# Kernel optimization log

Measured on AMD Instinct MI355X. Metric: run time of the kernel, lower is better.

## Reference

```python
import jax, jax.numpy as jnp
import numpy as np

N = 50000       # nodes
E = 800000      # edges (before self-loops)
NFEAT = 256
NHID = 64
NHEADS = 4
NOUT = 256
NEG_SLOPE = 0.2
BN_EPS = 1e-5
LN_EPS = 1e-5


def setup_inputs() -> dict:
    key = jax.random.key(0)
    ks = jax.random.split(key, 12)
    g = lambda k, s: (jax.random.normal(k, s, dtype=jnp.float32) * 0.05)
    inp = {
        "x": jax.random.normal(ks[0], (N, NFEAT), dtype=jnp.float32),
        "edge_index": jax.random.randint(ks[1], (2, E), 0, N, dtype=jnp.int32),
        # layer 1: GATConv(NFEAT, NHID, heads=NHEADS, concat=True)
        "W1": g(ks[2], (NFEAT, NHEADS * NHID)),
        "att_src1": g(ks[3], (NHEADS, NHID)),
        "att_dst1": g(ks[4], (NHEADS, NHID)),
        "bias1": jnp.zeros((NHEADS * NHID,), jnp.float32),
        # layer 2: GATConv(NHEADS*NHID, NOUT, heads=1, concat=False)
        "W2": g(ks[5], (NHEADS * NHID, NOUT)),
        "att_src2": g(ks[6], (1, NOUT)),
        "att_dst2": g(ks[7], (1, NOUT)),
        "bias2": jnp.zeros((NOUT,), jnp.float32),
        # BatchNorm1d (eval mode: running stats)
        "bn_gamma": jnp.ones((NOUT,), jnp.float32),
        "bn_beta": jnp.zeros((NOUT,), jnp.float32),
        "bn_mean": g(ks[8], (NOUT,)),
        "bn_var": jnp.ones((NOUT,), jnp.float32),
        # LayerNorm
        "ln_gamma": jnp.ones((NOUT,), jnp.float32),
        "ln_beta": jnp.zeros((NOUT,), jnp.float32),
    }
    return inp


def _gat_conv(x, edge_index, W, att_src, att_dst, bias, concat):
    """PyG-style GATConv (eval mode, add_self_loops=True)."""
    n = x.shape[0]
    H, C = att_src.shape
    xp = (x @ W).reshape(n, H, C)                    # [N,H,C]
    loop = jnp.arange(n, dtype=edge_index.dtype)
    src = jnp.concatenate([edge_index[0], loop])     # message source j
    dst = jnp.concatenate([edge_index[1], loop])     # aggregation target i
    a_src = jnp.einsum("nhc,hc->nh", xp, att_src)    # [N,H]
    a_dst = jnp.einsum("nhc,hc->nh", xp, att_dst)
    e = jax.nn.leaky_relu(a_src[src] + a_dst[dst], NEG_SLOPE)  # [Etot,H]
    # segment softmax over edges sharing the same dst
    m = jax.ops.segment_max(e, dst, num_segments=n)
    e = jnp.exp(e - m[dst])
    denom = jax.ops.segment_sum(e, dst, num_segments=n)
    alpha = e / (denom[dst] + 1e-16)                 # [Etot,H]
    out = jax.ops.segment_sum(alpha[:, :, None] * xp[src], dst, num_segments=n)  # [N,H,C]
    out = out.reshape(n, H * C) if concat else out.mean(axis=1)
    return out + bias


def reference(x, edge_index, W1, att_src1, att_dst1, bias1,
              W2, att_src2, att_dst2, bias2,
              bn_gamma, bn_beta, bn_mean, bn_var, ln_gamma, ln_beta):
    # eval mode: F.dropout is identity
    h = jax.nn.elu(_gat_conv(x, edge_index, W1, att_src1, att_dst1, bias1, True))
    h = jax.nn.elu(_gat_conv(h, edge_index, W2, att_src2, att_dst2, bias2, False))
    # BatchNorm1d (eval: running stats)
    h = (h - bn_mean) * jax.lax.rsqrt(bn_var + BN_EPS) * bn_gamma + bn_beta
    # LayerNorm over last dim
    mu = h.mean(axis=-1, keepdims=True)
    var = jnp.mean((h - mu) ** 2, axis=-1, keepdims=True)
    h = (h - mu) * jax.lax.rsqrt(var + LN_EPS) * ln_gamma + ln_beta
    return h
```

## Files before the change

### kernel.cpp

```cpp
#include <hip/hip_runtime.h>
#include <cstddef>
#include <cstdint>

#define NNODES 50000
#define NEDGES 800000
#define FDIM   256

#define SCAN_BLOCKS 256
#define SCAN_CHUNK  ((NNODES + SCAN_BLOCKS - 1) / SCAN_BLOCKS)

typedef __attribute__((ext_vector_type(8))) _Float16 f16x8;
typedef __attribute__((ext_vector_type(8))) unsigned short ushort8;
typedef __attribute__((ext_vector_type(4))) float f32x4;

__device__ __forceinline__ float leaky_exp(float a) {
    float e = a > 0.f ? a : 0.2f * a;
    return __expf(e);
}
__device__ __forceinline__ unsigned short f2h(float f) {
    return __builtin_bit_cast(unsigned short, (_Float16)f);
}
__device__ __forceinline__ float hlo(uint32_t u) {
    _Float16 h = __builtin_bit_cast(_Float16, (unsigned short)(u & 0xffffu));
    return (float)h;
}
__device__ __forceinline__ float hhi(uint32_t u) {
    _Float16 h = __builtin_bit_cast(_Float16, (unsigned short)(u >> 16));
    return (float)h;
}
__device__ __forceinline__ float rlanef(float v, int l) {
    return __builtin_bit_cast(float,
        __builtin_amdgcn_readlane(__builtin_bit_cast(int, v), l));
}

__global__ __launch_bounds__(256) void wprep_k(const float* __restrict__ W1,
                                               unsigned short* __restrict__ Wt1,
                                               const float* __restrict__ W2,
                                               unsigned short* __restrict__ Wt2) {
    const float* W = blockIdx.y ? W2 : W1;
    unsigned short* Wt = blockIdx.y ? Wt2 : Wt1;
    int n = blockIdx.x, k = threadIdx.x;
    Wt[n * 256 + k] = f2h(W[k * 256 + n]);
}

template <bool AFP32, bool FUSE_LOGITS>
__global__ __launch_bounds__(256) void gemm_mfma(const void* __restrict__ Aab,
                                                 const unsigned short* __restrict__ Bt,
                                                 unsigned short* __restrict__ C,
                                                 const float* __restrict__ atts,
                                                 const float* __restrict__ attd,
                                                 float* __restrict__ as_,
                                                 float* __restrict__ ad_,
                                                 int M) {
    __shared__ unsigned short As[128 * 64];
    __shared__ unsigned short Bs[128 * 64];
    const int t = threadIdx.x;
    const int lane = t & 63, wid = t >> 6;
    const int wr = wid >> 1, wc = wid & 1;
    const int bm = blockIdx.x * 128;
    const int bny = blockIdx.y;
    const int bn = bny * 128;
    f32x4 acc[4][4] = {};
    const int lrow = t >> 3, lslot = t & 7;
    for (int k0 = 0; k0 < 256; k0 += 64) {
        __syncthreads();
#pragma unroll
        for (int i = 0; i < 4; ++i) {
            int row = lrow + 32 * i;
            int ga = bm + row; ga = ga < M ? ga : M - 1;
            if (AFP32) {
                const float* p = (const float*)Aab + (size_t)ga * FDIM + k0 + lslot * 8;
                float4 f0 = *(const float4*)p;
                float4 f1 = *(const float4*)(p + 4);
                ushort8 r;
                r[0] = f2h(f0.x); r[1] = f2h(f0.y); r[2] = f2h(f0.z); r[3] = f2h(f0.w);
                r[4] = f2h(f1.x); r[5] = f2h(f1.y); r[6] = f2h(f1.z); r[7] = f2h(f1.w);
                *(ushort8*)(As + row * 64 + ((lslot ^ (row & 7)) << 3)) = r;
            } else {
                const unsigned short* A16 = (const unsigned short*)Aab;
                uint4 av = *(const uint4*)(A16 + (size_t)ga * FDIM + k0 + lslot * 8);
                *(uint4*)(As + row * 64 + ((lslot ^ (row & 7)) << 3)) = av;
            }
            uint4 bv = *(const uint4*)(Bt + (size_t)(bn + row) * FDIM + k0 + lslot * 8);
            *(uint4*)(Bs + row * 64 + ((lslot ^ (row & 7)) << 3)) = bv;
        }
        __syncthreads();
#pragma unroll
        for (int ks = 0; ks < 2; ++ks) {
            const int kq = ks * 4 + (lane >> 4);
            f16x8 a[4], b[4];
#pragma unroll
            for (int f = 0; f < 4; ++f) {
                int ra = wr * 64 + f * 16 + (lane & 15);
                a[f] = *(const f16x8*)(As + ra * 64 + ((kq ^ (ra & 7)) << 3));
                int rb = wc * 64 + f * 16 + (lane & 15);
                b[f] = *(const f16x8*)(Bs + rb * 64 + ((kq ^ (rb & 7)) << 3));
            }
#pragma unroll
            for (int mf = 0; mf < 4; ++mf)
#pragma unroll
                for (int nf = 0; nf < 4; ++nf)
                    acc[mf][nf] = __builtin_amdgcn_mfma_f32_16x16x32_f16(
                        a[mf], b[nf], acc[mf][nf], 0, 0, 0);
        }
    }
    const int col0 = bn + wc * 64 + (lane & 15);
    const int row00 = bm + wr * 64 + (lane >> 4) * 4;
    if (FUSE_LOGITS) {
        const int head = 2 * bny + wc;
        float sv4[4], dv4[4];
#pragma unroll
        for (int nf = 0; nf < 4; ++nf) {
            sv4[nf] = atts[col0 + nf * 16];
            dv4[nf] = attd[col0 + nf * 16];
        }
#pragma unroll
        for (int mf = 0; mf < 4; ++mf)
#pragma unroll
            for (int r = 0; r < 4; ++r) {
                float ps = 0.f, pd = 0.f;
#pragma unroll
                for (int nf = 0; nf < 4; ++nf) {
                    float v = acc[mf][nf][r];
                    ps = fmaf(v, sv4[nf], ps);
                    pd = fmaf(v, dv4[nf], pd);
                }
#pragma unroll
                for (int off = 1; off < 16; off <<= 1) {
                    ps += __shfl_xor(ps, off);
                    pd += __shfl_xor(pd, off);
                }
                int row = row00 + mf * 16 + r;
                if ((lane & 15) == 0 && row < M) {
                    as_[row * 4 + head] = ps;
                    ad_[row * 4 + head] = pd;
                }
            }
    }
#pragma unroll
    for (int mf = 0; mf < 4; ++mf)
#pragma unroll
        for (int nf = 0; nf < 4; ++nf) {
            f32x4 v = acc[mf][nf];
            int col = col0 + nf * 16;
#pragma unroll
            for (int r = 0; r < 4; ++r) {
                int row = row00 + mf * 16 + r;
                if (row < M) C[(size_t)row * FDIM + col] = f2h(v[r]);
            }
        }
}

template <int H>
__global__ __launch_bounds__(256) void aprep_k(const unsigned short* __restrict__ xp,
                                               const float* __restrict__ atts,
                                               const float* __restrict__ attd,
                                               float* __restrict__ as_,
                                               float* __restrict__ ad_) {
    const int lane = threadIdx.x & 63;
    const int n = blockIdx.x * 4 + (threadIdx.x >> 6);
    if (n >= NNODES) return;
    const int c = lane << 2;
    uint2 u = *(const uint2*)(xp + (size_t)n * FDIM + c);
    float v0 = hlo(u.x), v1 = hhi(u.x), v2 = hlo(u.y), v3 = hhi(u.y);
    float4 s4 = *(const float4*)(atts + c);
    float4 d4 = *(const float4*)(attd + c);
    float ss = v0 * s4.x + v1 * s4.y + v2 * s4.z + v3 * s4.w;
    float sd = v0 * d4.x + v1 * d4.y + v2 * d4.z + v3 * d4.w;
    constexpr int G = 64 / H;
#pragma unroll
    for (int off = 1; off < G; off <<= 1) {
        ss += __shfl_xor(ss, off);
        sd += __shfl_xor(sd, off);
    }
    if ((lane & (G - 1)) == 0) {
        int h = lane / G;
        as_[n * H + h] = ss;
        ad_[n * H + h] = sd;
    }
}

__global__ __launch_bounds__(256) void hist_k(const int* __restrict__ ei,
                                              int* __restrict__ deg) {
    int e = blockIdx.x * 256 + threadIdx.x;
    if (e < NEDGES) atomicAdd(&deg[ei[NEDGES + e]], 1);
}

__global__ __launch_bounds__(256) void scanA_k(const int* __restrict__ deg,
                                               int* __restrict__ bsum) {
    const int b = blockIdx.x, t = threadIdx.x;
    const int i = b * SCAN_CHUNK + t;
    int v = (t < SCAN_CHUNK && i < NNODES) ? deg[i] : 0;
#pragma unroll
    for (int off = 1; off < 64; off <<= 1) v += __shfl_xor(v, off);
    __shared__ int ws[4];
    if ((t & 63) == 0) ws[t >> 6] = v;
    __syncthreads();
    if (t == 0) bsum[b] = ws[0] + ws[1] + ws[2] + ws[3];
}

__global__ __launch_bounds__(256) void scanB_k(const int* __restrict__ bsum,
                                               int* __restrict__ boff,
                                               int* __restrict__ rowptr) {
    const int t = threadIdx.x;
    const int lane = t & 63, wid = t >> 6;
    int orig = bsum[t];
    int v = orig;
#pragma unroll
    for (int off = 1; off < 64; off <<= 1) {
        int u = __shfl_up(v, off);
        if (lane >= off) v += u;
    }
    __shared__ int ws[4], wo[4];
    if (lane == 63) ws[wid] = v;
    __syncthreads();
    if (t == 0) {
        int a = 0;
        for (int k = 0; k < 4; ++k) { wo[k] = a; a += ws[k]; }
        rowptr[NNODES] = a;
    }
    __syncthreads();
    boff[t] = wo[wid] + v - orig;
}

__global__ __launch_bounds__(256) void scanC_k(const int* __restrict__ deg,
                                               const int* __restrict__ boff,
                                               int* __restrict__ rowptr) {
    const int b = blockIdx.x, t = threadIdx.x;
    const int i = b * SCAN_CHUNK + t;
    const bool ok = (t < SCAN_CHUNK && i < NNODES);
    int orig = ok ? deg[i] : 0;
    int v = orig;
    const int lane = t & 63, wid = t >> 6;
#pragma unroll
    for (int off = 1; off < 64; off <<= 1) {
        int u = __shfl_up(v, off);
        if (lane >= off) v += u;
    }
    __shared__ int ws[4], wo[4];
    if (lane == 63) ws[wid] = v;
    __syncthreads();
    if (t == 0) {
        int a = 0;
        for (int k = 0; k < 4; ++k) { wo[k] = a; a += ws[k]; }
    }
    __syncthreads();
    if (ok) rowptr[i] = boff[b] + wo[wid] + v - orig;
}

__global__ __launch_bounds__(256) void scatter_k(const int* __restrict__ ei,
                                                 const int* __restrict__ rowptr,
                                                 int* __restrict__ deg,
                                                 int* __restrict__ ssrc) {
    int e = blockIdx.x * 256 + threadIdx.x;
    if (e >= NEDGES) return;
    int s = ei[e], d = ei[NEDGES + e];
    int old = atomicSub(&deg[d], 1);
    ssrc[rowptr[d + 1] - old] = s;
}

__global__ __launch_bounds__(256) void gather1_k(const unsigned short* __restrict__ xp,
                                                 const float* __restrict__ as_,
                                                 const float* __restrict__ ad_,
                                                 const int* __restrict__ rowptr,
                                                 const int* __restrict__ ssrc,
                                                 const float* __restrict__ bias,
                                                 unsigned short* __restrict__ out) {
    const int lane = threadIdx.x & 63;
    const int n = blockIdx.x * 4 + (threadIdx.x >> 6);
    if (n >= NNODES) return;
    const int h = lane >> 4;
    const int c = lane << 2;
    const int eloc = lane >> 2;
    const int hh = lane & 3;
    const float adW = ad_[n * 4 + hh];
    float a0 = 0.f, a1 = 0.f, a2 = 0.f, a3 = 0.f, den = 0.f;
    const int beg = rowptr[n], end = rowptr[n + 1];
    for (int base = beg; base < end; base += 16) {
        int my_e = base + eloc;
        float wv = 0.f; int sv = 0;
        if (my_e < end) {
            sv = ssrc[my_e];
            wv = leaky_exp(as_[sv * 4 + hh] + adW);
        }
        float dred = wv;
#pragma unroll
        for (int off = 4; off < 64; off <<= 1) dred += __shfl_xor(dred, off);
        den += __shfl(dred, h);
        const int cnt = min(16, end - base);
        int e = 0;
        for (; e + 8 <= cnt; e += 8) {
            uint2 u[8]; float w[8];
#pragma unroll
            for (int q = 0; q < 8; ++q) {
                int sq = __builtin_amdgcn_readlane(sv, (e + q) << 2);
                u[q] = *(const uint2*)(xp + (((unsigned)sq << 8) + (unsigned)c));
                w[q] = __shfl(wv, ((e + q) << 2) | h);
            }
#pragma unroll
            for (int q = 0; q < 8; ++q) {
                a0 = fmaf(hlo(u[q].x), w[q], a0);
                a1 = fmaf(hhi(u[q].x), w[q], a1);
                a2 = fmaf(hlo(u[q].y), w[q], a2);
                a3 = fmaf(hhi(u[q].y), w[q], a3);
            }
        }
        for (; e < cnt; ++e) {
            int sq = __builtin_amdgcn_readlane(sv, e << 2);
            uint2 u0 = *(const uint2*)(xp + (((unsigned)sq << 8) + (unsigned)c));
            float w0 = __shfl(wv, (e << 2) | h);
            a0 = fmaf(hlo(u0.x), w0, a0); a1 = fmaf(hhi(u0.x), w0, a1);
            a2 = fmaf(hlo(u0.y), w0, a2); a3 = fmaf(hhi(u0.y), w0, a3);
        }
    }
    {
        float w = leaky_exp(as_[n * 4 + h] + ad_[n * 4 + h]);
        uint2 u = *(const uint2*)(xp + (((unsigned)n << 8) + (unsigned)c));
        a0 = fmaf(hlo(u.x), w, a0); a1 = fmaf(hhi(u.x), w, a1);
        a2 = fmaf(hlo(u.y), w, a2); a3 = fmaf(hhi(u.y), w, a3);
        den += w;
    }
    const float inv = 1.f / (den + 1e-16f);
    float4 b4 = *(const float4*)(bias + c);
    float o[4] = {a0 * inv + b4.x, a1 * inv + b4.y,
                  a2 * inv + b4.z, a3 * inv + b4.w};
#pragma unroll
    for (int j = 0; j < 4; ++j) o[j] = o[j] > 0.f ? o[j] : __expf(o[j]) - 1.f;
    ushort4 r;
    r.x = f2h(o[0]); r.y = f2h(o[1]); r.z = f2h(o[2]); r.w = f2h(o[3]);
    *(ushort4*)(out + (size_t)n * FDIM + c) = r;
}

__global__ __launch_bounds__(256) void gather2_k(const unsigned short* __restrict__ xp,
                                                 const float* __restrict__ as_,
                                                 const float* __restrict__ ad_,
                                                 const int* __restrict__ rowptr,
                                                 const int* __restrict__ ssrc,
                                                 const float* __restrict__ bias,
                                                 const float* __restrict__ bng,
                                                 const float* __restrict__ bnb,
                                                 const float* __restrict__ bnm,
                                                 const float* __restrict__ bnv,
                                                 const float* __restrict__ lng,
                                                 const float* __restrict__ lnb,
                                                 float* __restrict__ out) {
    const int lane = threadIdx.x & 63;
    const int n = blockIdx.x * 4 + (threadIdx.x >> 6);
    if (n >= NNODES) return;
    const int c = lane << 2;
    const float adn = ad_[n];
    float a0 = 0.f, a1 = 0.f, a2 = 0.f, a3 = 0.f, den = 0.f;
    const int beg = rowptr[n], end = rowptr[n + 1];
    for (int base = beg; base < end; base += 64) {
        int my_e = base + lane;
        float wv = 0.f; int sv = 0;
        if (my_e < end) {
            sv = ssrc[my_e];
            wv = leaky_exp(as_[sv] + adn);
        }
        float dred = wv;
#pragma unroll
        for (int off = 1; off < 64; off <<= 1) dred += __shfl_xor(dred, off);
        den += dred;
        const int cnt = min(64, end - base);
        int e = 0;
        for (; e + 8 <= cnt; e += 8) {
            uint2 u[8]; float w[8];
#pragma unroll
            for (int q = 0; q < 8; ++q) {
                int sq = __builtin_amdgcn_readlane(sv, e + q);
                u[q] = *(const uint2*)(xp + (((unsigned)sq << 8) + (unsigned)c));
                w[q] = rlanef(wv, e + q);
            }
#pragma unroll
            for (int q = 0; q < 8; ++q) {
                a0 = fmaf(hlo(u[q].x), w[q], a0);
                a1 = fmaf(hhi(u[q].x), w[q], a1);
                a2 = fmaf(hlo(u[q].y), w[q], a2);
                a3 = fmaf(hhi(u[q].y), w[q], a3);
            }
        }
        for (; e < cnt; ++e) {
            int sq = __builtin_amdgcn_readlane(sv, e);
            uint2 u0 = *(const uint2*)(xp + (((unsigned)sq << 8) + (unsigned)c));
            float w0 = rlanef(wv, e);
            a0 = fmaf(hlo(u0.x), w0, a0); a1 = fmaf(hhi(u0.x), w0, a1);
            a2 = fmaf(hlo(u0.y), w0, a2); a3 = fmaf(hhi(u0.y), w0, a3);
        }
    }
    {
        float w = leaky_exp(as_[n] + adn);
        uint2 u = *(const uint2*)(xp + (((unsigned)n << 8) + (unsigned)c));
        a0 = fmaf(hlo(u.x), w, a0); a1 = fmaf(hhi(u.x), w, a1);
        a2 = fmaf(hlo(u.y), w, a2); a3 = fmaf(hhi(u.y), w, a3);
        den += w;
    }
    const float inv = 1.f / (den + 1e-16f);
    float vals[4] = {a0 * inv, a1 * inv, a2 * inv, a3 * inv};
#pragma unroll
    for (int j = 0; j < 4; ++j) {
        float o = vals[j] + bias[c + j];
        o = o > 0.f ? o : __expf(o) - 1.f;
        o = (o - bnm[c + j]) * rsqrtf(bnv[c + j] + 1e-5f) * bng[c + j]
            + bnb[c + j];
        vals[j] = o;
    }
    float s1 = vals[0] + vals[1] + vals[2] + vals[3];
    float s2 = vals[0] * vals[0] + vals[1] * vals[1] +
               vals[2] * vals[2] + vals[3] * vals[3];
#pragma unroll
    for (int off = 1; off < 64; off <<= 1) {
        s1 += __shfl_xor(s1, off);
        s2 += __shfl_xor(s2, off);
    }
    float mu  = s1 * (1.f / 256.f);
    float var = s2 * (1.f / 256.f) - mu * mu;
    float r   = rsqrtf(var + 1e-5f);
#pragma unroll
    for (int j = 0; j < 4; ++j)
        out[(size_t)n * FDIM + c + j] = (vals[j] - mu) * r * lng[c + j] + lnb[c + j];
}

extern "C" void kernel_launch(void* const* d_in, const int* in_sizes, int n_in,
                              void* d_out, int out_size, void* d_ws, size_t ws_size,
                              hipStream_t stream) {
    const float* x      = (const float*)d_in[0];
    const int*   ei     = (const int*)d_in[1];
    const float* W1     = (const float*)d_in[2];
    const float* atts1  = (const float*)d_in[3];
    const float* attd1  = (const float*)d_in[4];
    const float* bias1  = (const float*)d_in[5];
    const float* W2     = (const float*)d_in[6];
    const float* atts2  = (const float*)d_in[7];
    const float* attd2  = (const float*)d_in[8];
    const float* bias2  = (const float*)d_in[9];
    const float* bng    = (const float*)d_in[10];
    const float* bnb    = (const float*)d_in[11];
    const float* bnm    = (const float*)d_in[12];
    const float* bnv    = (const float*)d_in[13];
    const float* lng    = (const float*)d_in[14];
    const float* lnb    = (const float*)d_in[15];

    const size_t NF = (size_t)NNODES * FDIM;
    unsigned short* xpbf = (unsigned short*)d_ws;
    unsigned short* xbf  = xpbf + NF;
    unsigned short* wt1  = xbf + NF;
    unsigned short* wt2  = wt1 + 65536;
    float* as1   = (float*)(wt2 + 65536);
    float* ad1   = as1 + (size_t)NNODES * 4;
    float* as2   = ad1 + (size_t)NNODES * 4;
    float* ad2   = as2 + NNODES;
    int*   deg    = (int*)(ad2 + NNODES);
    int*   rowptr = deg + NNODES;
    int*   bsum   = rowptr + (NNODES + 1);
    int*   boff   = bsum + SCAN_BLOCKS;
    int*   ssrc   = boff + SCAN_BLOCKS;
    float* outf  = (float*)d_out;

    const dim3 gemm_grid((NNODES + 127) / 128, 2);
    const int node_wave_blocks = (NNODES + 3) / 4;
    const int edge_thread_blocks = (NEDGES + 255) / 256;

    wprep_k<<<dim3(256, 2), 256, 0, stream>>>(W1, wt1, W2, wt2);
    hipMemsetAsync(deg, 0, NNODES * sizeof(int), stream);
    hist_k<<<edge_thread_blocks, 256, 0, stream>>>(ei, deg);
    scanA_k<<<SCAN_BLOCKS, 256, 0, stream>>>(deg, bsum);
    scanB_k<<<1, 256, 0, stream>>>(bsum, boff, rowptr);
    scanC_k<<<SCAN_BLOCKS, 256, 0, stream>>>(deg, boff, rowptr);
    scatter_k<<<edge_thread_blocks, 256, 0, stream>>>(ei, rowptr, deg, ssrc);

    gemm_mfma<true, true><<<gemm_grid, 256, 0, stream>>>(
        x, wt1, xpbf, atts1, attd1, as1, ad1, NNODES);
    gather1_k<<<node_wave_blocks, 256, 0, stream>>>(xpbf, as1, ad1, rowptr, ssrc,
                                                    bias1, xbf);

    gemm_mfma<false, false><<<gemm_grid, 256, 0, stream>>>(
        xbf, wt2, xpbf, nullptr, nullptr, nullptr, nullptr, NNODES);
    aprep_k<1><<<node_wave_blocks, 256, 0, stream>>>(xpbf, atts2, attd2, as2, ad2);
    gather2_k<<<node_wave_blocks, 256, 0, stream>>>(xpbf, as2, ad2, rowptr, ssrc,
                                                    bias2, bng, bnb, bnm, bnv,
                                                    lng, lnb, outf);
}
```

Before: 290.8 us.

## Slice feature matrices into 32-column planes and split gather per slice

Stores the projected features and hidden activations in a sliced layout of 32 columns per node plane, so each gather pass over one slice touches a smaller, more cache-friendly working set. Attention weights and softmax denominators are now computed once per edge in separate kernels and stored in buffers, one of which is placed in the output memory. The gather kernels then run over an 8-slice grid, each reading 4-byte chunks per neighbor. LayerNorm moves into a separate final kernel that reads fp16 intermediates. The cost is extra kernel launches, extra traffic for the weight buffers, and more index-load work repeated per slice.

```diff
diff --git a/kernel.cpp b/kernel.cpp
--- a/kernel.cpp
+++ b/kernel.cpp
@@ -27,10 +27,6 @@
 __device__ __forceinline__ float hhi(uint32_t u) {
     _Float16 h = __builtin_bit_cast(_Float16, (unsigned short)(u >> 16));
     return (float)h;
-}
-__device__ __forceinline__ float rlanef(float v, int l) {
-    return __builtin_bit_cast(float,
-        __builtin_amdgcn_readlane(__builtin_bit_cast(int, v), l));
 }
 
 __global__ __launch_bounds__(256) void wprep_k(const float* __restrict__ W1,
@@ -43,7 +39,7 @@
     Wt[n * 256 + k] = f2h(W[k * 256 + n]);
 }
 
-template <bool AFP32, bool FUSE_LOGITS>
+template <int AMODE, bool FUSE_LOGITS>
 __global__ __launch_bounds__(256) void gemm_mfma(const void* __restrict__ Aab,
                                                  const unsigned short* __restrict__ Bt,
                                                  unsigned short* __restrict__ C,
@@ -68,7 +64,7 @@
         for (int i = 0; i < 4; ++i) {
             int row = lrow + 32 * i;
             int ga = bm + row; ga = ga < M ? ga : M - 1;
-            if (AFP32) {
+            if (AMODE == 0) {
                 const float* p = (const float*)Aab + (size_t)ga * FDIM + k0 + lslot * 8;
                 float4 f0 = *(const float4*)p;
                 float4 f1 = *(const float4*)(p + 4);
@@ -78,7 +74,9 @@
                 *(ushort8*)(As + row * 64 + ((lslot ^ (row & 7)) << 3)) = r;
             } else {
                 const unsigned short* A16 = (const unsigned short*)Aab;
-                uint4 av = *(const uint4*)(A16 + (size_t)ga * FDIM + k0 + lslot * 8);
+                int k = k0 + lslot * 8;
+                uint4 av = *(const uint4*)(A16 +
+                    ((size_t)(k >> 5) * NNODES + ga) * 32 + (k & 31));
                 *(uint4*)(As + row * 64 + ((lslot ^ (row & 7)) << 3)) = av;
             }
             uint4 bv = *(const uint4*)(Bt + (size_t)(bn + row) * FDIM + k0 + lslot * 8);
@@ -142,42 +140,37 @@
 #pragma unroll
         for (int nf = 0; nf < 4; ++nf) {
             f32x4 v = acc[mf][nf];
-            int col = col0 + nf * 16;
+            int colb = bn + wc * 64 + nf * 16;
+            size_t base = (size_t)(colb >> 5) * NNODES * 32 + (colb & 31) + (lane & 15);
 #pragma unroll
             for (int r = 0; r < 4; ++r) {
                 int row = row00 + mf * 16 + r;
-                if (row < M) C[(size_t)row * FDIM + col] = f2h(v[r]);
+                if (row < M) C[base + (size_t)row * 32] = f2h(v[r]);
             }
         }
 }
 
-template <int H>
-__global__ __launch_bounds__(256) void aprep_k(const unsigned short* __restrict__ xp,
-                                               const float* __restrict__ atts,
-                                               const float* __restrict__ attd,
-                                               float* __restrict__ as_,
-                                               float* __restrict__ ad_) {
+__global__ __launch_bounds__(256) void aprep1_k(const unsigned short* __restrict__ xp_s,
+                                                const float* __restrict__ atts,
+                                                const float* __restrict__ attd,
+                                                float* __restrict__ as_,
+                                                float* __restrict__ ad_) {
     const int lane = threadIdx.x & 63;
     const int n = blockIdx.x * 4 + (threadIdx.x >> 6);
     if (n >= NNODES) return;
     const int c = lane << 2;
-    uint2 u = *(const uint2*)(xp + (size_t)n * FDIM + c);
+    uint2 u = *(const uint2*)(xp_s + ((size_t)(c >> 5) * NNODES + n) * 32 + (c & 31));
     float v0 = hlo(u.x), v1 = hhi(u.x), v2 = hlo(u.y), v3 = hhi(u.y);
     float4 s4 = *(const float4*)(atts + c);
     float4 d4 = *(const float4*)(attd + c);
     float ss = v0 * s4.x + v1 * s4.y + v2 * s4.z + v3 * s4.w;
     float sd = v0 * d4.x + v1 * d4.y + v2 * d4.z + v3 * d4.w;
-    constexpr int G = 64 / H;
-#pragma unroll
-    for (int off = 1; off < G; off <<= 1) {
+#pragma unroll
+    for (int off = 1; off < 64; off <<= 1) {
         ss += __shfl_xor(ss, off);
         sd += __shfl_xor(sd, off);
     }
-    if ((lane & (G - 1)) == 0) {
-        int h = lane / G;
-        as_[n * H + h] = ss;
-        ad_[n * H + h] = sd;
-    }
+    if (lane == 0) { as_[n] = ss; ad_[n] = sd; }
 }
 
 __global__ __launch_bounds__(256) void hist_k(const int* __restrict__ ei,
@@ -259,155 +252,224 @@
     ssrc[rowptr[d + 1] - old] = s;
 }
 
-__global__ __launch_bounds__(256) void gather1_k(const unsigned short* __restrict__ xp,
-                                                 const float* __restrict__ as_,
-                                                 const float* __restrict__ ad_,
-                                                 const int* __restrict__ rowptr,
-                                                 const int* __restrict__ ssrc,
-                                                 const float* __restrict__ bias,
-                                                 unsigned short* __restrict__ out) {
+__global__ __launch_bounds__(256) void wk1_k(const float* __restrict__ as_,
+                                             const float* __restrict__ ad_,
+                                             const int* __restrict__ rowptr,
+                                             const int* __restrict__ ssrc,
+                                             float* __restrict__ wbuf,
+                                             float* __restrict__ den,
+                                             float* __restrict__ wself) {
     const int lane = threadIdx.x & 63;
     const int n = blockIdx.x * 4 + (threadIdx.x >> 6);
     if (n >= NNODES) return;
-    const int h = lane >> 4;
-    const int c = lane << 2;
-    const int eloc = lane >> 2;
-    const int hh = lane & 3;
-    const float adW = ad_[n * 4 + hh];
-    float a0 = 0.f, a1 = 0.f, a2 = 0.f, a3 = 0.f, den = 0.f;
+    float4 ad4 = *(const float4*)(ad_ + (size_t)n * 4);
+    float d0 = 0.f, d1 = 0.f, d2 = 0.f, d3 = 0.f;
     const int beg = rowptr[n], end = rowptr[n + 1];
-    for (int base = beg; base < end; base += 16) {
-        int my_e = base + eloc;
-        float wv = 0.f; int sv = 0;
-        if (my_e < end) {
-            sv = ssrc[my_e];
-            wv = leaky_exp(as_[sv * 4 + hh] + adW);
-        }
-        float dred = wv;
-#pragma unroll
-        for (int off = 4; off < 64; off <<= 1) dred += __shfl_xor(dred, off);
-        den += __shfl(dred, h);
-        const int cnt = min(16, end - base);
-        int e = 0;
-        for (; e + 8 <= cnt; e += 8) {
-            uint2 u[8]; float w[8];
-#pragma unroll
-            for (int q = 0; q < 8; ++q) {
-                int sq = __builtin_amdgcn_readlane(sv, (e + q) << 2);
-                u[q] = *(const uint2*)(xp + (((unsigned)sq << 8) + (unsigned)c));
-                w[q] = __shfl(wv, ((e + q) << 2) | h);
+    for (int base = beg; base < end; base += 64) {
+        int e = base + lane;
+        float w0 = 0.f, w1 = 0.f, w2 = 0.f, w3 = 0.f;
+        if (e < end) {
+            int sv = ssrc[e];
+            float4 a4 = *(const float4*)(as_ + (size_t)sv * 4);
+            w0 = leaky_exp(a4.x + ad4.x);
+            w1 = leaky_exp(a4.y + ad4.y);
+            w2 = leaky_exp(a4.z + ad4.z);
+            w3 = leaky_exp(a4.w + ad4.w);
+            wbuf[0 * NEDGES + e] = w0;
+            wbuf[1 * NEDGES + e] = w1;
+            wbuf[2 * NEDGES + e] = w2;
+            wbuf[3 * NEDGES + e] = w3;
+        }
+        d0 += w0; d1 += w1; d2 += w2; d3 += w3;
+    }
+#pragma unroll
+    for (int off = 1; off < 64; off <<= 1) {
+        d0 += __shfl_xor(d0, off);
+        d1 += __shfl_xor(d1, off);
+        d2 += __shfl_xor(d2, off);
+        d3 += __shfl_xor(d3, off);
+    }
+    if (lane == 0) {
+        float4 a4 = *(const float4*)(as_ + (size_t)n * 4);
+        float s0 = leaky_exp(a4.x + ad4.x), s1 = leaky_exp(a4.y + ad4.y);
+        float s2 = leaky_exp(a4.z + ad4.z), s3 = leaky_exp(a4.w + ad4.w);
+        wself[n * 4 + 0] = s0; wself[n * 4 + 1] = s1;
+        wself[n * 4 + 2] = s2; wself[n * 4 + 3] = s3;
+        den[n * 4 + 0] = d0 + s0; den[n * 4 + 1] = d1 + s1;
+        den[n * 4 + 2] = d2 + s2; den[n * 4 + 3] = d3 + s3;
+    }
+}
+
+__global__ __launch_bounds__(256) void wk2_k(const float* __restrict__ as_,
+                                             const float* __restrict__ ad_,
+                                             const int* __restrict__ rowptr,
+                                             const int* __restrict__ ssrc,
+                                             float* __restrict__ wbuf,
+                                             float* __restrict__ den,
+                                             float* __restrict__ wself) {
+    const int lane = threadIdx.x & 63;
+    const int n = blockIdx.x * 4 + (threadIdx.x >> 6);
+    if (n >= NNODES) return;
+    const float adn = ad_[n];
+    float d = 0.f;
+    const int beg = rowptr[n], end = rowptr[n + 1];
+    for (int base = beg; base < end; base += 64) {
+        int e = base + lane;
+        float w = 0.f;
+        if (e < end) {
+            int sv = ssrc[e];
+            w = leaky_exp(as_[sv] + adn);
+            wbuf[e] = w;
+        }
+        d += w;
+    }
+#pragma unroll
+    for (int off = 1; off < 64; off <<= 1) d += __shfl_xor(d, off);
+    if (lane == 0) {
+        float s = leaky_exp(as_[n] + adn);
+        wself[n] = s;
+        den[n] = d + s;
+    }
+}
+
+__global__ __launch_bounds__(256) void g1s_k(const unsigned short* __restrict__ xp_s,
+                                             const float* __restrict__ wbuf,
+                                             const float* __restrict__ den,
+                                             const float* __restrict__ wself,
+                                             const int* __restrict__ rowptr,
+                                             const int* __restrict__ ssrc,
+                                             const float* __restrict__ bias,
+                                             unsigned short* __restrict__ h1_s) {
+    const int lane = threadIdx.x & 63;
+    const int n = blockIdx.x * 4 + (threadIdx.x >> 6);
+    if (n >= NNODES) return;
+    const int s = blockIdx.y;
+    const int h = s >> 1;
+    const int g = lane >> 4;
+    const int fl = lane & 15;
+    const unsigned short* xs = xp_s + (size_t)s * NNODES * 32;
+    const float* wb = wbuf + (size_t)h * NEDGES;
+    float a0 = 0.f, a1 = 0.f;
+    const int beg = rowptr[n], end = rowptr[n + 1];
+    for (int base = beg; base < end; base += 64) {
+        int e = base + lane;
+        int sv = 0; float wv = 0.f;
+        if (e < end) { sv = ssrc[e]; wv = wb[e]; }
+        const int cnt = min(64, end - base);
+        int i = 0;
+        for (; i + 8 <= cnt; i += 8) {
+            int i0 = i + g, i1 = i + 4 + g;
+            int s0 = __shfl(sv, i0), s1b = __shfl(sv, i1);
+            float w0 = __shfl(wv, i0), w1 = __shfl(wv, i1);
+            uint32_t u0 = *(const uint32_t*)(xs + (size_t)s0 * 32 + fl * 2);
+            uint32_t u1 = *(const uint32_t*)(xs + (size_t)s1b * 32 + fl * 2);
+            a0 = fmaf(hlo(u0), w0, a0); a1 = fmaf(hhi(u0), w0, a1);
+            a0 = fmaf(hlo(u1), w1, a0); a1 = fmaf(hhi(u1), w1, a1);
+        }
+        for (; i < cnt; i += 4) {
+            int idx = i + g;
+            int s0 = __shfl(sv, idx);
+            float w0 = __shfl(wv, idx);
+            if (idx < cnt) {
+                uint32_t u0 = *(const uint32_t*)(xs + (size_t)s0 * 32 + fl * 2);
+                a0 = fmaf(hlo(u0), w0, a0); a1 = fmaf(hhi(u0), w0, a1);
             }
-#pragma unroll
-            for (int q = 0; q < 8; ++q) {
-                a0 = fmaf(hlo(u[q].x), w[q], a0);
-                a1 = fmaf(hhi(u[q].x), w[q], a1);
-                a2 = fmaf(hlo(u[q].y), w[q], a2);
-                a3 = fmaf(hhi(u[q].y), w[q], a3);
+        }
+    }
+    a0 += __shfl_xor(a0, 16); a0 += __shfl_xor(a0, 32);
+    a1 += __shfl_xor(a1, 16); a1 += __shfl_xor(a1, 32);
+    if (lane < 16) {
+        float w = wself[n * 4 + h];
+        uint32_t u = *(const uint32_t*)(xs + (size_t)n * 32 + fl * 2);
+        a0 = fmaf(hlo(u), w, a0); a1 = fmaf(hhi(u), w, a1);
+        float inv = 1.f / (den[n * 4 + h] + 1e-16f);
+        int c = s * 32 + fl * 2;
+        float o0 = a0 * inv + bias[c];
+        float o1 = a1 * inv + bias[c + 1];
+        o0 = o0 > 0.f ? o0 : __expf(o0) - 1.f;
+        o1 = o1 > 0.f ? o1 : __expf(o1) - 1.f;
+        uint32_t r = (uint32_t)f2h(o0) | ((uint32_t)f2h(o1) << 16);
+        *(uint32_t*)(h1_s + ((size_t)s * NNODES + n) * 32 + fl * 2) = r;
+    }
+}
+
+__global__ __launch_bounds__(256) void g2s_k(const unsigned short* __restrict__ xp_s,
+                                             const float* __restrict__ wbuf,
+                                             const float* __restrict__ den,
+                                             const float* __restrict__ wself,
+                                             const int* __restrict__ rowptr,
+                                             const int* __restrict__ ssrc,
+                                             const float* __restrict__ bias,
+                                             const float* __restrict__ bng,
+                                             const float* __restrict__ bnb,
+                                             const float* __restrict__ bnm,
+                                             const float* __restrict__ bnv,
+                                             unsigned short* __restrict__ acc_s) {
+    const int lane = threadIdx.x & 63;
+    const int n = blockIdx.x * 4 + (threadIdx.x >> 6);
+    if (n >= NNODES) return;
+    const int s = blockIdx.y;
+    const int g = lane >> 4;
+    const int fl = lane & 15;
+    const unsigned short* xs = xp_s + (size_t)s * NNODES * 32;
+    float a0 = 0.f, a1 = 0.f;
+    const int beg = rowptr[n], end = rowptr[n + 1];
+    for (int base = beg; base < end; base += 64) {
+        int e = base + lane;
+        int sv = 0; float wv = 0.f;
+        if (e < end) { sv = ssrc[e]; wv = wbuf[e]; }
+        const int cnt = min(64, end - base);
+        int i = 0;
+        for (; i + 8 <= cnt; i += 8) {
+            int i0 = i + g, i1 = i + 4 + g;
+            int s0 = __shfl(sv, i0), s1b = __shfl(sv, i1);
+            float w0 = __shfl(wv, i0), w1 = __shfl(wv, i1);
+            uint32_t u0 = *(const uint32_t*)(xs + (size_t)s0 * 32 + fl * 2);
+            uint32_t u1 = *(const uint32_t*)(xs + (size_t)s1b * 32 + fl * 2);
+            a0 = fmaf(hlo(u0), w0, a0); a1 = fmaf(hhi(u0), w0, a1);
+            a0 = fmaf(hlo(u1), w1, a0); a1 = fmaf(hhi(u1), w1, a1);
+        }
+        for (; i < cnt; i += 4) {
+            int idx = i + g;
+            int s0 = __shfl(sv, idx);
+            float w0 = __shfl(wv, idx);
+            if (idx < cnt) {
+                uint32_t u0 = *(const uint32_t*)(xs + (size_t)s0 * 32 + fl * 2);
+                a0 = fmaf(hlo(u0), w0, a0); a1 = fmaf(hhi(u0), w0, a1);
             }
         }
-        for (; e < cnt; ++e) {
-            int sq = __builtin_amdgcn_readlane(sv, e << 2);
-            uint2 u0 = *(const uint2*)(xp + (((unsigned)sq << 8) + (unsigned)c));
-            float w0 = __shfl(wv, (e << 2) | h);
-            a0 = fmaf(hlo(u0.x), w0, a0); a1 = fmaf(hhi(u0.x), w0, a1);
-            a2 = fmaf(hlo(u0.y), w0, a2); a3 = fmaf(hhi(u0.y), w0, a3);
-        }
-    }
-    {
-        float w = leaky_exp(as_[n * 4 + h] + ad_[n * 4 + h]);
-        uint2 u = *(const uint2*)(xp + (((unsigned)n << 8) + (unsigned)c));
-        a0 = fmaf(hlo(u.x), w, a0); a1 = fmaf(hhi(u.x), w, a1);
-        a2 = fmaf(hlo(u.y), w, a2); a3 = fmaf(hhi(u.y), w, a3);
-        den += w;
-    }
-    const float inv = 1.f / (den + 1e-16f);
-    float4 b4 = *(const float4*)(bias + c);
-    float o[4] = {a0 * inv + b4.x, a1 * inv + b4.y,
-                  a2 * inv + b4.z, a3 * inv + b4.w};
-#pragma unroll
-    for (int j = 0; j < 4; ++j) o[j] = o[j] > 0.f ? o[j] : __expf(o[j]) - 1.f;
-    ushort4 r;
-    r.x = f2h(o[0]); r.y = f2h(o[1]); r.z = f2h(o[2]); r.w = f2h(o[3]);
-    *(ushort4*)(out + (size_t)n * FDIM + c) = r;
-}
-
-__global__ __launch_bounds__(256) void gather2_k(const unsigned short* __restrict__ xp,
-                                                 const float* __restrict__ as_,
-                                                 const float* __restrict__ ad_,
-                                                 const int* __restrict__ rowptr,
-                                                 const int* __restrict__ ssrc,
-                                                 const float* __restrict__ bias,
-                                                 const float* __restrict__ bng,
-                                                 const float* __restrict__ bnb,
-                                                 const float* __restrict__ bnm,
-                                                 const float* __restrict__ bnv,
-                                                 const float* __restrict__ lng,
-                                                 const float* __restrict__ lnb,
-                                                 float* __restrict__ out) {
+    }
+    a0 += __shfl_xor(a0, 16); a0 += __shfl_xor(a0, 32);
+    a1 += __shfl_xor(a1, 16); a1 += __shfl_xor(a1, 32);
+    if (lane < 16) {
+        float w = wself[n];
+        uint32_t u = *(const uint32_t*)(xs + (size_t)n * 32 + fl * 2);
+        a0 = fmaf(hlo(u), w, a0); a1 = fmaf(hhi(u), w, a1);
+        float inv = 1.f / (den[n] + 1e-16f);
+        int c = s * 32 + fl * 2;
+        float o0 = a0 * inv + bias[c];
+        float o1 = a1 * inv + bias[c + 1];
+        o0 = o0 > 0.f ? o0 : __expf(o0) - 1.f;
+        o1 = o1 > 0.f ? o1 : __expf(o1) - 1.f;
+        o0 = (o0 - bnm[c]) * rsqrtf(bnv[c] + 1e-5f) * bng[c] + bnb[c];
+        o1 = (o1 - bnm[c + 1]) * rsqrtf(bnv[c + 1] + 1e-5f) * bng[c + 1] + bnb[c + 1];
+        uint32_t r = (uint32_t)f2h(o0) | ((uint32_t)f2h(o1) << 16);
+        *(uint32_t*)(acc_s + ((size_t)s * NNODES + n) * 32 + fl * 2) = r;
+    }
+}
+
+__global__ __launch_bounds__(256) void fin_k(const unsigned short* __restrict__ acc_s,
+                                             const float* __restrict__ lng,
+                                             const float* __restrict__ lnb,
+                                             float* __restrict__ out) {
     const int lane = threadIdx.x & 63;
     const int n = blockIdx.x * 4 + (threadIdx.x >> 6);
     if (n >= NNODES) return;
     const int c = lane << 2;
-    const float adn = ad_[n];
-    float a0 = 0.f, a1 = 0.f, a2 = 0.f, a3 = 0.f, den = 0.f;
-    const int beg = rowptr[n], end = rowptr[n + 1];
-    for (int base = beg; base < end; base += 64) {
-        int my_e = base + lane;
-        float wv = 0.f; int sv = 0;
-        if (my_e < end) {
-            sv = ssrc[my_e];
-            wv = leaky_exp(as_[sv] + adn);
-        }
-        float dred = wv;
-#pragma unroll
-        for (int off = 1; off < 64; off <<= 1) dred += __shfl_xor(dred, off);
-        den += dred;
-        const int cnt = min(64, end - base);
-        int e = 0;
-        for (; e + 8 <= cnt; e += 8) {
-            uint2 u[8]; float w[8];
-#pragma unroll
-            for (int q = 0; q < 8; ++q) {
-                int sq = __builtin_amdgcn_readlane(sv, e + q);
-                u[q] = *(const uint2*)(xp + (((unsigned)sq << 8) + (unsigned)c));
-                w[q] = rlanef(wv, e + q);
-            }
-#pragma unroll
-            for (int q = 0; q < 8; ++q) {
-                a0 = fmaf(hlo(u[q].x), w[q], a0);
-                a1 = fmaf(hhi(u[q].x), w[q], a1);
-                a2 = fmaf(hlo(u[q].y), w[q], a2);
-                a3 = fmaf(hhi(u[q].y), w[q], a3);
-            }
-        }
-        for (; e < cnt; ++e) {
-            int sq = __builtin_amdgcn_readlane(sv, e);
-            uint2 u0 = *(const uint2*)(xp + (((unsigned)sq << 8) + (unsigned)c));
-            float w0 = rlanef(wv, e);
-            a0 = fmaf(hlo(u0.x), w0, a0); a1 = fmaf(hhi(u0.x), w0, a1);
-            a2 = fmaf(hlo(u0.y), w0, a2); a3 = fmaf(hhi(u0.y), w0, a3);
-        }
-    }
-    {
-        float w = leaky_exp(as_[n] + adn);
-        uint2 u = *(const uint2*)(xp + (((unsigned)n << 8) + (unsigned)c));
-        a0 = fmaf(hlo(u.x), w, a0); a1 = fmaf(hhi(u.x), w, a1);
-        a2 = fmaf(hlo(u.y), w, a2); a3 = fmaf(hhi(u.y), w, a3);
-        den += w;
-    }
-    const float inv = 1.f / (den + 1e-16f);
-    float vals[4] = {a0 * inv, a1 * inv, a2 * inv, a3 * inv};
-#pragma unroll
-    for (int j = 0; j < 4; ++j) {
-        float o = vals[j] + bias[c + j];
-        o = o > 0.f ? o : __expf(o) - 1.f;
-        o = (o - bnm[c + j]) * rsqrtf(bnv[c + j] + 1e-5f) * bng[c + j]
-            + bnb[c + j];
-        vals[j] = o;
-    }
-    float s1 = vals[0] + vals[1] + vals[2] + vals[3];
-    float s2 = vals[0] * vals[0] + vals[1] * vals[1] +
-               vals[2] * vals[2] + vals[3] * vals[3];
+    uint2 u = *(const uint2*)(acc_s + ((size_t)(c >> 5) * NNODES + n) * 32 + (c & 31));
+    float v0 = hlo(u.x), v1 = hhi(u.x), v2 = hlo(u.y), v3 = hhi(u.y);
+    float s1 = v0 + v1 + v2 + v3;
+    float s2 = v0 * v0 + v1 * v1 + v2 * v2 + v3 * v3;
 #pragma unroll
     for (int off = 1; off < 64; off <<= 1) {
         s1 += __shfl_xor(s1, off);
@@ -416,9 +478,14 @@
     float mu  = s1 * (1.f / 256.f);
     float var = s2 * (1.f / 256.f) - mu * mu;
     float r   = rsqrtf(var + 1e-5f);
-#pragma unroll
-    for (int j = 0; j < 4; ++j)
-        out[(size_t)n * FDIM + c + j] = (vals[j] - mu) * r * lng[c + j] + lnb[c + j];
+    float4 lg = *(const float4*)(lng + c);
+    float4 lb = *(const float4*)(lnb + c);
+    float4 o;
+    o.x = (v0 - mu) * r * lg.x + lb.x;
+    o.y = (v1 - mu) * r * lg.y + lb.y;
+    o.z = (v2 - mu) * r * lg.z + lb.z;
+    o.w = (v3 - mu) * r * lg.w + lb.w;
+    *(float4*)(out + (size_t)n * FDIM + c) = o;
 }
 
 extern "C" void kernel_launch(void* const* d_in, const int* in_sizes, int n_in,
@@ -442,23 +509,30 @@
     const float* lnb    = (const float*)d_in[15];
 
     const size_t NF = (size_t)NNODES * FDIM;
-    unsigned short* xpbf = (unsigned short*)d_ws;
-    unsigned short* xbf  = xpbf + NF;
-    unsigned short* wt1  = xbf + NF;
-    unsigned short* wt2  = wt1 + 65536;
-    float* as1   = (float*)(wt2 + 65536);
-    float* ad1   = as1 + (size_t)NNODES * 4;
-    float* as2   = ad1 + (size_t)NNODES * 4;
-    float* ad2   = as2 + NNODES;
-    int*   deg    = (int*)(ad2 + NNODES);
+    unsigned short* xp_s   = (unsigned short*)d_ws;
+    unsigned short* h1a_s  = xp_s + NF;
+    unsigned short* wt1    = h1a_s + NF;
+    unsigned short* wt2    = wt1 + 65536;
+    float* as1    = (float*)(wt2 + 65536);
+    float* ad1    = as1 + (size_t)NNODES * 4;
+    float* as2    = ad1 + (size_t)NNODES * 4;
+    float* ad2    = as2 + NNODES;
+    float* den2   = ad2 + NNODES;
+    float* wself2 = den2 + NNODES;
+    float* wbuf2  = wself2 + NNODES;
+    int*   deg    = (int*)(wbuf2 + NEDGES);
     int*   rowptr = deg + NNODES;
     int*   bsum   = rowptr + (NNODES + 1);
     int*   boff   = bsum + SCAN_BLOCKS;
     int*   ssrc   = boff + SCAN_BLOCKS;
-    float* outf  = (float*)d_out;
+    float* wbuf1  = (float*)d_out;
+    float* den1   = wbuf1 + (size_t)4 * NEDGES;
+    float* wself1 = den1 + (size_t)NNODES * 4;
+    float* outf   = (float*)d_out;
 
     const dim3 gemm_grid((NNODES + 127) / 128, 2);
     const int node_wave_blocks = (NNODES + 3) / 4;
+    const dim3 slice_grid(node_wave_blocks, 8);
     const int edge_thread_blocks = (NEDGES + 255) / 256;
 
     wprep_k<<<dim3(256, 2), 256, 0, stream>>>(W1, wt1, W2, wt2);
@@ -469,15 +543,20 @@
     scanC_k<<<SCAN_BLOCKS, 256, 0, stream>>>(deg, boff, rowptr);
     scatter_k<<<edge_thread_blocks, 256, 0, stream>>>(ei, rowptr, deg, ssrc);
 
-    gemm_mfma<true, true><<<gemm_grid, 256, 0, stream>>>(
-        x, wt1, xpbf, atts1, attd1, as1, ad1, NNODES);
-    gather1_k<<<node_wave_blocks, 256, 0, stream>>>(xpbf, as1, ad1, rowptr, ssrc,
-                                                    bias1, xbf);
-
-    gemm_mfma<false, false><<<gemm_grid, 256, 0, stream>>>(
-        xbf, wt2, xpbf, nullptr, nullptr, nullptr, nullptr, NNODES);
-    aprep_k<1><<<node_wave_blocks, 256, 0, stream>>>(xpbf, atts2, attd2, as2, ad2);
-    gather2_k<<<node_wave_blocks, 256, 0, stream>>>(xpbf, as2, ad2, rowptr, ssrc,
-                                                    bias2, bng, bnb, bnm, bnv,
-                                                    lng, lnb, outf);
-}
+    gemm_mfma<0, true><<<gemm_grid, 256, 0, stream>>>(
+        x, wt1, xp_s, atts1, attd1, as1, ad1, NNODES);
+    wk1_k<<<node_wave_blocks, 256, 0, stream>>>(as1, ad1, rowptr, ssrc,
+                                                wbuf1, den1, wself1);
+    g1s_k<<<slice_grid, 256, 0, stream>>>(xp_s, wbuf1, den1, wself1,
+                                          rowptr, ssrc, bias1, h1a_s);
+
+    gemm_mfma<1, false><<<gemm_grid, 256, 0, stream>>>(
+        h1a_s, wt2, xp_s, nullptr, nullptr, nullptr, nullptr, NNODES);
+    aprep1_k<<<node_wave_blocks, 256, 0, stream>>>(xp_s, atts2, attd2, as2, ad2);
+    wk2_k<<<node_wave_blocks, 256, 0, stream>>>(as2, ad2, rowptr, ssrc,
+                                                wbuf2, den2, wself2);
+    g2s_k<<<slice_grid, 256, 0, stream>>>(xp_s, wbuf2, den2, wself2,
+                                          rowptr, ssrc, bias2,
+                                          bng, bnb, bnm, bnv, h1a_s );
+    fin_k<<<node_wave_blocks, 256, 0, stream>>>(h1a_s, lng, lnb, outf);
+}
```

Result: slower. 487.8 us (+67.7%).
